# Kernel optimization log

Measured on AMD Instinct MI355X. Metric: run time of the kernel, lower is better.

## Reference

```python
import jax, jax.numpy as jnp
import numpy as np

B, Q, K, DQ, DK, H, DV = 4, 512, 512, 512, 512, 256, 512


def setup_inputs() -> dict:
    key = jax.random.key(0)
    ks = jax.random.split(key, 9)
    return {
        "query": jax.random.normal(ks[0], (B, Q, DQ), dtype=jnp.float32),
        "key": jax.random.normal(ks[1], (B, K, DK), dtype=jnp.float32),
        "value": jax.random.normal(ks[2], (B, K, DV), dtype=jnp.float32),
        "Wq": jax.random.normal(ks[3], (DQ, H), dtype=jnp.float32) / np.sqrt(DQ),
        "bq": jax.random.normal(ks[4], (H,), dtype=jnp.float32) * 0.01,
        "Wk": jax.random.normal(ks[5], (DK, H), dtype=jnp.float32) / np.sqrt(DK),
        "bk": jax.random.normal(ks[6], (H,), dtype=jnp.float32) * 0.01,
        "wv": jax.random.normal(ks[7], (H,), dtype=jnp.float32) / np.sqrt(H),
        "bv": jax.random.normal(ks[8], (), dtype=jnp.float32) * 0.01,
    }


def reference(query, key, value, Wq, bq, Wk, bk, wv, bv):
    # Projections: [B,Q,H] and [B,K,H]
    q = jnp.einsum("bqd,dh->bqh", query, Wq) + bq
    k = jnp.einsum("bkd,dh->bkh", key, Wk) + bk
    # Broadcast add + tanh: [B,Q,K,H] (the large intermediate)
    feat = jnp.tanh(q[:, :, None, :] + k[:, None, :, :])
    # Linear-to-scalar score: [B,Q,K]
    score = jnp.einsum("bqkh,h->bqk", feat, wv) + bv
    attention_weight = jax.nn.softmax(score, axis=-1)
    # Dropout is identity at eval; weighted sum over keys: [B,Q,DV]
    context = jnp.einsum("bqk,bkd->bqd", attention_weight, value)
    return (context, attention_weight)
```

## Files before the change

### kernel.cpp

```cpp
#include <hip/hip_runtime.h>
#include <hip/hip_bf16.h>

#define B_ 4
#define Q_ 512
#define K_ 512
#define DQ_ 512
#define H_ 256
#define DV_ 512

#define SC2 2.8853900817779268f

typedef unsigned short u16;
typedef short bf16x8 __attribute__((ext_vector_type(8)));
typedef float f32x4 __attribute__((ext_vector_type(4)));
typedef float f32x2 __attribute__((ext_vector_type(2)));
typedef unsigned short u16x4 __attribute__((ext_vector_type(4)));

__device__ __forceinline__ unsigned bsplit(float a) {
    unsigned u  = __float_as_uint(a);
    unsigned hi = (u + 0x7FFFu + ((u >> 16) & 1u)) >> 16;
    float hf = __uint_as_float(hi << 16);
    float l  = a - hf;
    unsigned ul = __float_as_uint(l);
    unsigned lo = (ul + 0x7FFFu + ((ul >> 16) & 1u)) >> 16;
    return (hi << 16) | lo;
}

__device__ __forceinline__ void gld16(const void* g, void* l) {
    __builtin_amdgcn_global_load_lds(
        (const __attribute__((address_space(1))) unsigned int*)g,
        (__attribute__((address_space(3))) unsigned int*)l, 16, 0, 0);
}

__device__ __forceinline__ void pair_acc(
    f32x2 Eq0, f32x2 Eq1, float ek0, float ek1,
    float w0, float w1, float w01, f32x2& acc)
{
    f32x2 e0 = Eq0 * (f32x2){ek0, ek0};
    f32x2 e1 = Eq1 * (f32x2){ek1, ek1};
    f32x2 s  = e0 + e1;
    f32x2 den = __builtin_elementwise_fma(e0, e1, s);
    den = den + (f32x2){1.f, 1.f};
    f32x2 num = __builtin_elementwise_fma(e1, (f32x2){w0, w0}, (f32x2){w01, w01});
    num = __builtin_elementwise_fma(e0, (f32x2){w1, w1}, num);
    f32x2 r = {__builtin_amdgcn_rcpf(den.x), __builtin_amdgcn_rcpf(den.y)};
    acc = __builtin_elementwise_fma(num, r, acc);
}

__global__ __launch_bounds__(256) void cvt_rows(
    const float* __restrict__ query, const float* __restrict__ key,
    u16* __restrict__ qA_hi, u16* __restrict__ qA_lo)
{
    const int z = blockIdx.y;
    const float* src = z ? key : query;
    u16* dh = qA_hi + (long long)z * 1048576;
    u16* dl = qA_lo + (long long)z * 1048576;
    long long i4 = (long long)blockIdx.x * 256 + threadIdx.x;
    float4 v = ((const float4*)src)[i4];
    unsigned a = bsplit(v.x), b = bsplit(v.y), c = bsplit(v.z), d = bsplit(v.w);
    u16x4 h4 = {(u16)(a >> 16), (u16)(b >> 16), (u16)(c >> 16), (u16)(d >> 16)};
    u16x4 l4 = {(u16)(a & 0xFFFF), (u16)(b & 0xFFFF), (u16)(c & 0xFFFF), (u16)(d & 0xFFFF)};
    *(u16x4*)(dh + i4 * 4) = h4;
    *(u16x4*)(dl + i4 * 4) = l4;
}

__global__ __launch_bounds__(256) void cvt_T(
    const float* __restrict__ Wq, const float* __restrict__ Wk,
    const float* __restrict__ value,
    u16* __restrict__ WT_hi, u16* __restrict__ WT_lo,
    u16* __restrict__ vT_hi, u16* __restrict__ vT_lo)
{
    __shared__ float t[32][33];
    const int z = blockIdx.z;
    const int x = threadIdx.x, y = threadIdx.y;
    const float* src; u16 *dh, *dl; int C;
    if (z < 2) {
        if (blockIdx.y >= 8) return;
        src = z ? Wk : Wq; C = 256;
        dh = WT_hi + (long long)z * 131072;
        dl = WT_lo + (long long)z * 131072;
    } else {
        src = value + (long long)(z - 2) * 262144; C = 512;
        dh = vT_hi + (long long)(z - 2) * 262144;
        dl = vT_lo + (long long)(z - 2) * 262144;
    }
    const int r0 = blockIdx.x * 32, c0 = blockIdx.y * 32;
    #pragma unroll
    for (int i = 0; i < 32; i += 8)
        t[y + i][x] = src[(long long)(r0 + y + i) * C + c0 + x];
    __syncthreads();
    #pragma unroll
    for (int i = 0; i < 32; i += 8) {
        unsigned p = bsplit(t[x][y + i]);
        long long o = (long long)(c0 + y + i) * 512 + r0 + x;
        dh[o] = (u16)(p >> 16);
        dl[o] = (u16)(p & 0xFFFF);
    }
}

__global__ __launch_bounds__(256) void mfma_gemm(
    const u16* __restrict__ Ah0, const u16* __restrict__ Al0,
    const u16* __restrict__ Bh0, const u16* __restrict__ Bl0,
    const float* __restrict__ biasq, const float* __restrict__ biask,
    float* __restrict__ outp, int mode, int Kd,
    long long sA, long long sB, long long sO)
{
    const int z = blockIdx.z;
    const u16* Ah = Ah0 + z * sA;
    const u16* Al = Al0 + z * sA;
    const u16* Bh = Bh0 + z * sB;
    const u16* Bl = Bl0 + z * sB;

    const int m0 = blockIdx.x * 64;
    const int n0 = blockIdx.y * 64;

    __shared__ u16 AhS[64 * 64], AlS[64 * 64], BhS[64 * 64], BlS[64 * 64];

    const int tid = threadIdx.x;
    const int lane = tid & 63, w = tid >> 6;
    const int wr = w >> 1, wc = w & 1;
    const int lrow = lane & 15, lgrp = lane >> 4;

    f32x4 acc[2][2] = {};

    for (int k0 = 0; k0 < Kd; k0 += 64) {
        #pragma unroll
        for (int it = 0; it < 2; ++it) {
            int idx = tid + it * 256;
            int row = idx >> 3, u = idx & 7;
            long long go = (long long)(m0 + row) * Kd + k0 + ((u ^ (row & 7)) << 3);
            long long gb = (long long)(n0 + row) * Kd + k0 + ((u ^ (row & 7)) << 3);
            gld16(Ah + go, AhS + idx * 8);
            gld16(Al + go, AlS + idx * 8);
            gld16(Bh + gb, BhS + idx * 8);
            gld16(Bl + gb, BlS + idx * 8);
        }
        __syncthreads();

        #pragma unroll
        for (int kk = 0; kk < 2; ++kk) {
            bf16x8 ah[2], al[2], bh[2], bl[2];
            #pragma unroll
            for (int f = 0; f < 2; ++f) {
                int ar = wr * 32 + f * 16 + lrow;
                int au = (kk * 4 + lgrp) ^ (ar & 7);
                ah[f] = *(const bf16x8*)(AhS + ar * 64 + au * 8);
                al[f] = *(const bf16x8*)(AlS + ar * 64 + au * 8);
                int br = wc * 32 + f * 16 + lrow;
                int bu = (kk * 4 + lgrp) ^ (br & 7);
                bh[f] = *(const bf16x8*)(BhS + br * 64 + bu * 8);
                bl[f] = *(const bf16x8*)(BlS + br * 64 + bu * 8);
            }
            #pragma unroll
            for (int fm = 0; fm < 2; ++fm)
                #pragma unroll
                for (int fn = 0; fn < 2; ++fn) {
                    acc[fm][fn] = __builtin_amdgcn_mfma_f32_16x16x32_bf16(ah[fm], bh[fn], acc[fm][fn], 0, 0, 0);
                    acc[fm][fn] = __builtin_amdgcn_mfma_f32_16x16x32_bf16(ah[fm], bl[fn], acc[fm][fn], 0, 0, 0);
                    acc[fm][fn] = __builtin_amdgcn_mfma_f32_16x16x32_bf16(al[fm], bh[fn], acc[fm][fn], 0, 0, 0);
                }
        }
        __syncthreads();
    }

    if (mode == 0) {
        const float* bs = z ? biask : biasq;
        #pragma unroll
        for (int fm = 0; fm < 2; ++fm)
            #pragma unroll
            for (int fn = 0; fn < 2; ++fn)
                #pragma unroll
                for (int r = 0; r < 4; ++r) {
                    int m = m0 + wr * 32 + fm * 16 + lgrp * 4 + r;
                    int n = n0 + wc * 32 + fn * 16 + lrow;
                    float v = __builtin_amdgcn_exp2f((acc[fm][fn][r] + bs[n]) * SC2);
                    if (z == 0) {
                        outp[(((long long)(m >> 2) * H_ + n) << 2) + (m & 3)] = v;
                    } else {
                        int bb = m >> 9, k = m & 511;
                        outp[sO + (((long long)(bb * 64 + (n >> 2)) * 512 + k) << 2) + (n & 3)] = v;
                    }
                }
    } else {
        float* C = outp + (long long)z * sO;
        #pragma unroll
        for (int fm = 0; fm < 2; ++fm)
            #pragma unroll
            for (int fn = 0; fn < 2; ++fn)
                #pragma unroll
                for (int r = 0; r < 4; ++r) {
                    int m = m0 + wr * 32 + fm * 16 + lgrp * 4 + r;
                    int n = n0 + wc * 32 + fn * 16 + lrow;
                    C[(long long)m * DV_ + n] = acc[fm][fn][r];
                }
    }
}

#define QT 4

__global__ __launch_bounds__(1024) void score_softmax(
    const float* __restrict__ qp4E,
    const float* __restrict__ kT4E,
    const float* __restrict__ wv,
    float* __restrict__ attn_out,
    u16* __restrict__ aB_hi, u16* __restrict__ aB_lo)
{
    const int b   = blockIdx.y;
    const int q0  = blockIdx.x * QT;
    const int tid = threadIdx.x;
    const int k16 = tid & 255;
    const int qtr = tid >> 8;
    const int lane = tid & 63;

    __shared__ float lq[H_][QT];
    __shared__ float lwp[H_ / 2][4];
    __shared__ float pacc[3][2][256][4];
    __shared__ float red[4][QT];

    if (tid < H_) {
        const float4* qsrc = (const float4*)qp4E + ((long long)(b * (Q_ / 4) + blockIdx.x)) * H_;
        *(float4*)&lq[tid][0] = qsrc[tid];
    } else if (tid < H_ + H_ / 2) {
        int p = tid - H_;
        float w0 = wv[2 * p], w1 = wv[2 * p + 1];
        lwp[p][0] = w0; lwp[p][1] = w1; lwp[p][2] = w0 + w1; lwp[p][3] = 0.f;
    }
    __syncthreads();

    f32x2 a01[2] = {{0.f,0.f},{0.f,0.f}}, a23[2] = {{0.f,0.f},{0.f,0.f}};
    const float4* kvec = (const float4*)kT4E + (long long)b * (H_ / 4) * K_ + k16;
    const int g0 = qtr * 16;

    float4 kA = kvec[(long long)g0 * K_];
    float4 kB = kvec[(long long)g0 * K_ + 256];
    #pragma unroll 2
    for (int gi = 0; gi < 16; ++gi) {
        const int g = g0 + gi;
        float4 kAc = kA, kBc = kB;
        if (gi < 15) {
            kA = kvec[(long long)(g + 1) * K_];
            kB = kvec[(long long)(g + 1) * K_ + 256];
        }
        float4 q4_0 = *(const float4*)&lq[(g << 2) + 0][0];
        float4 q4_1 = *(const float4*)&lq[(g << 2) + 1][0];
        float4 q4_2 = *(const float4*)&lq[(g << 2) + 2][0];
        float4 q4_3 = *(const float4*)&lq[(g << 2) + 3][0];
        float4 wp0 = *(const float4*)&lwp[(g << 1) + 0][0];
        float4 wp1 = *(const float4*)&lwp[(g << 1) + 1][0];

        f32x2 q0_01 = {q4_0.x, q4_0.y}, q0_23 = {q4_0.z, q4_0.w};
        f32x2 q1_01 = {q4_1.x, q4_1.y}, q1_23 = {q4_1.z, q4_1.w};
        f32x2 q2_01 = {q4_2.x, q4_2.y}, q2_23 = {q4_2.z, q4_2.w};
        f32x2 q3_01 = {q4_3.x, q4_3.y}, q3_23 = {q4_3.z, q4_3.w};

        pair_acc(q0_01, q1_01, kAc.x, kAc.y, wp0.x, wp0.y, wp0.z, a01[0]);
        pair_acc(q0_23, q1_23, kAc.x, kAc.y, wp0.x, wp0.y, wp0.z, a23[0]);
        pair_acc(q2_01, q3_01, kAc.z, kAc.w, wp1.x, wp1.y, wp1.z, a01[0]);
        pair_acc(q2_23, q3_23, kAc.z, kAc.w, wp1.x, wp1.y, wp1.z, a23[0]);
        pair_acc(q0_01, q1_01, kBc.x, kBc.y, wp0.x, wp0.y, wp0.z, a01[1]);
        pair_acc(q0_23, q1_23, kBc.x, kBc.y, wp0.x, wp0.y, wp0.z, a23[1]);
        pair_acc(q2_01, q3_01, kBc.z, kBc.w, wp1.x, wp1.y, wp1.z, a01[1]);
        pair_acc(q2_23, q3_23, kBc.z, kBc.w, wp1.x, wp1.y, wp1.z, a23[1]);
    }

    if (qtr) {
        #pragma unroll
        for (int kk = 0; kk < 2; ++kk) {
            float4 v = make_float4(a01[kk].x, a01[kk].y, a23[kk].x, a23[kk].y);
            *(float4*)&pacc[qtr - 1][kk][k16][0] = v;
        }
    }
    __syncthreads();

    float s[2][QT], e[2][QT], mx[QT];
    if (!qtr) {
        #pragma unroll
        for (int kk = 0; kk < 2; ++kk) {
            float4 t0 = *(const float4*)&pacc[0][kk][k16][0];
            float4 t1 = *(const float4*)&pacc[1][kk][k16][0];
            float4 t2 = *(const float4*)&pacc[2][kk][k16][0];
            s[kk][0] = -2.f * (a01[kk].x + t0.x + t1.x + t2.x);
            s[kk][1] = -2.f * (a01[kk].y + t0.y + t1.y + t2.y);
            s[kk][2] = -2.f * (a23[kk].x + t0.z + t1.z + t2.z);
            s[kk][3] = -2.f * (a23[kk].y + t0.w + t1.w + t2.w);
        }
        #pragma unroll
        for (int qq = 0; qq < QT; ++qq) {
            float v = fmaxf(s[0][qq], s[1][qq]);
            #pragma unroll
            for (int off = 32; off; off >>= 1) v = fmaxf(v, __shfl_xor(v, off));
            if (lane == 0) red[tid >> 6][qq] = v;
        }
    }
    __syncthreads();
    if (!qtr) {
        #pragma unroll
        for (int qq = 0; qq < QT; ++qq)
            mx[qq] = fmaxf(fmaxf(red[0][qq], red[1][qq]), fmaxf(red[2][qq], red[3][qq]));
    }
    __syncthreads();
    if (!qtr) {
        #pragma unroll
        for (int qq = 0; qq < QT; ++qq) {
            e[0][qq] = __expf(s[0][qq] - mx[qq]);
            e[1][qq] = __expf(s[1][qq] - mx[qq]);
            float v = e[0][qq] + e[1][qq];
            #pragma unroll
            for (int off = 32; off; off >>= 1) v += __shfl_xor(v, off);
            if (lane == 0) red[tid >> 6][qq] = v;
        }
    }
    __syncthreads();
    if (!qtr) {
        #pragma unroll
        for (int qq = 0; qq < QT; ++qq) {
            float v = red[0][qq] + red[1][qq] + red[2][qq] + red[3][qq];
            float rv = __builtin_amdgcn_rcpf(v);
            #pragma unroll
            for (int kk = 0; kk < 2; ++kk) {
                float a = e[kk][qq] * rv;
                long long o = (long long)(b * Q_ + q0 + qq) * K_ + k16 + kk * 256;
                attn_out[o] = a;
                unsigned p = bsplit(a);
                aB_hi[o] = (u16)(p >> 16);
                aB_lo[o] = (u16)(p & 0xFFFF);
            }
        }
    }
}

extern "C" void kernel_launch(void* const* d_in, const int* in_sizes, int n_in,
                              void* d_out, int out_size, void* d_ws, size_t ws_size,
                              hipStream_t stream) {
    const float* query = (const float*)d_in[0];
    const float* key   = (const float*)d_in[1];
    const float* value = (const float*)d_in[2];
    const float* Wq    = (const float*)d_in[3];
    const float* bq    = (const float*)d_in[4];
    const float* Wk    = (const float*)d_in[5];
    const float* bk    = (const float*)d_in[6];
    const float* wv    = (const float*)d_in[7];

    float* out = (float*)d_out;
    float* ctx_out  = out;
    float* attn_out = out + (size_t)B_ * Q_ * DV_;

    float* ws   = (float*)d_ws;
    float* qp4  = ws;
    float* kT4  = qp4 + 524288;
    u16* qA_hi  = (u16*)(kT4 + 524288);
    u16* kA_hi  = qA_hi + 1048576;
    u16* qA_lo  = kA_hi + 1048576;
    u16* kA_lo  = qA_lo + 1048576;
    u16* WqT_hi = kA_lo + 1048576;
    u16* WkT_hi = WqT_hi + 131072;
    u16* WqT_lo = WkT_hi + 131072;
    u16* WkT_lo = WqT_lo + 131072;
    u16* vT_hi  = WkT_lo + 131072;
    u16* vT_lo  = vT_hi + 1048576;
    u16* aB_hi  = vT_lo + 1048576;
    u16* aB_lo  = aB_hi + 1048576;
    (void)qA_lo; (void)WqT_lo; (void)n_in; (void)ws_size; (void)in_sizes; (void)out_size;

    hipLaunchKernelGGL(cvt_rows, dim3(1024, 2), dim3(256), 0, stream,
                       query, key, qA_hi, qA_lo);
    hipLaunchKernelGGL(cvt_T, dim3(16, 16, 6), dim3(32, 8), 0, stream,
                       Wq, Wk, value, WqT_hi, WqT_lo, vT_hi, vT_lo);

    hipLaunchKernelGGL(mfma_gemm, dim3(32, 4, 2), dim3(256), 0, stream,
                       qA_hi, qA_lo, WqT_hi, WqT_lo, bq, bk, qp4, 0, 512,
                       (long long)1048576, (long long)131072, (long long)524288);

    hipLaunchKernelGGL(score_softmax, dim3(Q_ / QT, B_), dim3(1024), 0, stream,
                       qp4, kT4, wv, attn_out, aB_hi, aB_lo);

    hipLaunchKernelGGL(mfma_gemm, dim3(8, 8, 4), dim3(256), 0, stream,
                       aB_hi, aB_lo, vT_hi, vT_lo, (const float*)nullptr, (const float*)nullptr,
                       ctx_out, 2, 512,
                       (long long)262144, (long long)262144, (long long)262144);
}
```

Before: 72.59 us.

## Merge conversion kernels, vectorize transpose stores, drop softmax max pass

Result: faster. 65.79 us (-9.4%).

```diff
diff --git a/kernel.cpp b/kernel.cpp
--- a/kernel.cpp
+++ b/kernel.cpp
@@ -47,35 +47,41 @@
     acc = __builtin_elementwise_fma(num, r, acc);
 }
 
-__global__ __launch_bounds__(256) void cvt_rows(
+__global__ __launch_bounds__(256) void prep_all(
     const float* __restrict__ query, const float* __restrict__ key,
-    u16* __restrict__ qA_hi, u16* __restrict__ qA_lo)
-{
-    const int z = blockIdx.y;
-    const float* src = z ? key : query;
-    u16* dh = qA_hi + (long long)z * 1048576;
-    u16* dl = qA_lo + (long long)z * 1048576;
-    long long i4 = (long long)blockIdx.x * 256 + threadIdx.x;
-    float4 v = ((const float4*)src)[i4];
-    unsigned a = bsplit(v.x), b = bsplit(v.y), c = bsplit(v.z), d = bsplit(v.w);
-    u16x4 h4 = {(u16)(a >> 16), (u16)(b >> 16), (u16)(c >> 16), (u16)(d >> 16)};
-    u16x4 l4 = {(u16)(a & 0xFFFF), (u16)(b & 0xFFFF), (u16)(c & 0xFFFF), (u16)(d & 0xFFFF)};
-    *(u16x4*)(dh + i4 * 4) = h4;
-    *(u16x4*)(dl + i4 * 4) = l4;
-}
-
-__global__ __launch_bounds__(256) void cvt_T(
     const float* __restrict__ Wq, const float* __restrict__ Wk,
     const float* __restrict__ value,
+    u16* __restrict__ qA_hi, u16* __restrict__ qA_lo,
     u16* __restrict__ WT_hi, u16* __restrict__ WT_lo,
     u16* __restrict__ vT_hi, u16* __restrict__ vT_lo)
 {
+    const int bx  = blockIdx.x;
+    const int tid = threadIdx.x;
+
+    if (bx < 2048) {
+        const int z = bx >> 10;
+        const float* src = z ? key : query;
+        u16* dh = qA_hi + (long long)z * 1048576;
+        u16* dl = qA_lo + (long long)z * 1048576;
+        long long i4 = (long long)(bx & 1023) * 256 + tid;
+        float4 v = ((const float4*)src)[i4];
+        unsigned a = bsplit(v.x), b = bsplit(v.y), c = bsplit(v.z), d = bsplit(v.w);
+        u16x4 h4 = {(u16)(a >> 16), (u16)(b >> 16), (u16)(c >> 16), (u16)(d >> 16)};
+        u16x4 l4 = {(u16)(a & 0xFFFF), (u16)(b & 0xFFFF), (u16)(c & 0xFFFF), (u16)(d & 0xFFFF)};
+        *(u16x4*)(dh + i4 * 4) = h4;
+        *(u16x4*)(dl + i4 * 4) = l4;
+        return;
+    }
+
     __shared__ float t[32][33];
-    const int z = blockIdx.z;
-    const int x = threadIdx.x, y = threadIdx.y;
+    const int flat = bx - 2048;
+    const int z  = flat >> 8;
+    const int rem = flat & 255;
+    const int gx = rem & 15, gy = rem >> 4;
+    const int x = tid & 31, y = tid >> 5;
     const float* src; u16 *dh, *dl; int C;
     if (z < 2) {
-        if (blockIdx.y >= 8) return;
+        if (gy >= 8) return;
         src = z ? Wk : Wq; C = 256;
         dh = WT_hi + (long long)z * 131072;
         dl = WT_lo + (long long)z * 131072;
@@ -84,17 +90,22 @@
         dh = vT_hi + (long long)(z - 2) * 262144;
         dl = vT_lo + (long long)(z - 2) * 262144;
     }
-    const int r0 = blockIdx.x * 32, c0 = blockIdx.y * 32;
+    const int r0 = gx * 32, c0 = gy * 32;
     #pragma unroll
     for (int i = 0; i < 32; i += 8)
         t[y + i][x] = src[(long long)(r0 + y + i) * C + c0 + x];
     __syncthreads();
-    #pragma unroll
-    for (int i = 0; i < 32; i += 8) {
-        unsigned p = bsplit(t[x][y + i]);
-        long long o = (long long)(c0 + y + i) * 512 + r0 + x;
-        dh[o] = (u16)(p >> 16);
-        dl[o] = (u16)(p & 0xFFFF);
+    {
+        const int r = tid >> 3, c = tid & 7;
+        unsigned p0 = bsplit(t[4 * c + 0][r]);
+        unsigned p1 = bsplit(t[4 * c + 1][r]);
+        unsigned p2 = bsplit(t[4 * c + 2][r]);
+        unsigned p3 = bsplit(t[4 * c + 3][r]);
+        long long o = (long long)(c0 + r) * 512 + r0 + 4 * c;
+        u16x4 h4 = {(u16)(p0 >> 16), (u16)(p1 >> 16), (u16)(p2 >> 16), (u16)(p3 >> 16)};
+        u16x4 l4 = {(u16)(p0 & 0xFFFF), (u16)(p1 & 0xFFFF), (u16)(p2 & 0xFFFF), (u16)(p3 & 0xFFFF)};
+        *(u16x4*)(dh + o) = h4;
+        *(u16x4*)(dl + o) = l4;
     }
 }
 
@@ -231,37 +242,52 @@
     const float4* kvec = (const float4*)kT4E + (long long)b * (H_ / 4) * K_ + k16;
     const int g0 = qtr * 16;
 
-    float4 kA = kvec[(long long)g0 * K_];
-    float4 kB = kvec[(long long)g0 * K_ + 256];
-    #pragma unroll 2
-    for (int gi = 0; gi < 16; ++gi) {
-        const int g = g0 + gi;
-        float4 kAc = kA, kBc = kB;
-        if (gi < 15) {
-            kA = kvec[(long long)(g + 1) * K_];
-            kB = kvec[(long long)(g + 1) * K_ + 256];
-        }
-        float4 q4_0 = *(const float4*)&lq[(g << 2) + 0][0];
-        float4 q4_1 = *(const float4*)&lq[(g << 2) + 1][0];
-        float4 q4_2 = *(const float4*)&lq[(g << 2) + 2][0];
-        float4 q4_3 = *(const float4*)&lq[(g << 2) + 3][0];
-        float4 wp0 = *(const float4*)&lwp[(g << 1) + 0][0];
-        float4 wp1 = *(const float4*)&lwp[(g << 1) + 1][0];
-
-        f32x2 q0_01 = {q4_0.x, q4_0.y}, q0_23 = {q4_0.z, q4_0.w};
-        f32x2 q1_01 = {q4_1.x, q4_1.y}, q1_23 = {q4_1.z, q4_1.w};
-        f32x2 q2_01 = {q4_2.x, q4_2.y}, q2_23 = {q4_2.z, q4_2.w};
-        f32x2 q3_01 = {q4_3.x, q4_3.y}, q3_23 = {q4_3.z, q4_3.w};
-
-        pair_acc(q0_01, q1_01, kAc.x, kAc.y, wp0.x, wp0.y, wp0.z, a01[0]);
-        pair_acc(q0_23, q1_23, kAc.x, kAc.y, wp0.x, wp0.y, wp0.z, a23[0]);
-        pair_acc(q2_01, q3_01, kAc.z, kAc.w, wp1.x, wp1.y, wp1.z, a01[0]);
-        pair_acc(q2_23, q3_23, kAc.z, kAc.w, wp1.x, wp1.y, wp1.z, a23[0]);
-        pair_acc(q0_01, q1_01, kBc.x, kBc.y, wp0.x, wp0.y, wp0.z, a01[1]);
-        pair_acc(q0_23, q1_23, kBc.x, kBc.y, wp0.x, wp0.y, wp0.z, a23[1]);
-        pair_acc(q2_01, q3_01, kBc.z, kBc.w, wp1.x, wp1.y, wp1.z, a01[1]);
-        pair_acc(q2_23, q3_23, kBc.z, kBc.w, wp1.x, wp1.y, wp1.z, a23[1]);
-    }
+#define SCORE_COMPUTE(GI, kAc, kBc) do {                                        \
+        const int g_ = g0 + (GI);                                               \
+        float4 q4_0 = *(const float4*)&lq[(g_ << 2) + 0][0];                    \
+        float4 q4_1 = *(const float4*)&lq[(g_ << 2) + 1][0];                    \
+        float4 q4_2 = *(const float4*)&lq[(g_ << 2) + 2][0];                    \
+        float4 q4_3 = *(const float4*)&lq[(g_ << 2) + 3][0];                    \
+        float4 wp0 = *(const float4*)&lwp[(g_ << 1) + 0][0];                    \
+        float4 wp1 = *(const float4*)&lwp[(g_ << 1) + 1][0];                    \
+        f32x2 q0_01 = {q4_0.x, q4_0.y}, q0_23 = {q4_0.z, q4_0.w};               \
+        f32x2 q1_01 = {q4_1.x, q4_1.y}, q1_23 = {q4_1.z, q4_1.w};               \
+        f32x2 q2_01 = {q4_2.x, q4_2.y}, q2_23 = {q4_2.z, q4_2.w};               \
+        f32x2 q3_01 = {q4_3.x, q4_3.y}, q3_23 = {q4_3.z, q4_3.w};               \
+        pair_acc(q0_01, q1_01, (kAc).x, (kAc).y, wp0.x, wp0.y, wp0.z, a01[0]);  \
+        pair_acc(q0_23, q1_23, (kAc).x, (kAc).y, wp0.x, wp0.y, wp0.z, a23[0]);  \
+        pair_acc(q2_01, q3_01, (kAc).z, (kAc).w, wp1.x, wp1.y, wp1.z, a01[0]);  \
+        pair_acc(q2_23, q3_23, (kAc).z, (kAc).w, wp1.x, wp1.y, wp1.z, a23[0]);  \
+        pair_acc(q0_01, q1_01, (kBc).x, (kBc).y, wp0.x, wp0.y, wp0.z, a01[1]);  \
+        pair_acc(q0_23, q1_23, (kBc).x, (kBc).y, wp0.x, wp0.y, wp0.z, a23[1]);  \
+        pair_acc(q2_01, q3_01, (kBc).z, (kBc).w, wp1.x, wp1.y, wp1.z, a01[1]);  \
+        pair_acc(q2_23, q3_23, (kBc).z, (kBc).w, wp1.x, wp1.y, wp1.z, a23[1]);  \
+    } while (0)
+
+    float4 A0 = kvec[(long long)(g0 + 0) * K_];
+    float4 B0 = kvec[(long long)(g0 + 0) * K_ + 256];
+    float4 A1 = kvec[(long long)(g0 + 1) * K_];
+    float4 B1 = kvec[(long long)(g0 + 1) * K_ + 256];
+    #pragma unroll
+    for (int gi = 0; gi < 16; gi += 2) {
+        {
+            float4 kAc = A0, kBc = B0;
+            if (gi + 2 < 16) {
+                A0 = kvec[(long long)(g0 + gi + 2) * K_];
+                B0 = kvec[(long long)(g0 + gi + 2) * K_ + 256];
+            }
+            SCORE_COMPUTE(gi, kAc, kBc);
+        }
+        {
+            float4 kAc = A1, kBc = B1;
+            if (gi + 3 < 16) {
+                A1 = kvec[(long long)(g0 + gi + 3) * K_];
+                B1 = kvec[(long long)(g0 + gi + 3) * K_ + 256];
+            }
+            SCORE_COMPUTE(gi + 1, kAc, kBc);
+        }
+    }
+#undef SCORE_COMPUTE
 
     if (qtr) {
         #pragma unroll
@@ -272,38 +298,24 @@
     }
     __syncthreads();
 
-    float s[2][QT], e[2][QT], mx[QT];
+    float e[2][QT];
     if (!qtr) {
         #pragma unroll
         for (int kk = 0; kk < 2; ++kk) {
             float4 t0 = *(const float4*)&pacc[0][kk][k16][0];
             float4 t1 = *(const float4*)&pacc[1][kk][k16][0];
             float4 t2 = *(const float4*)&pacc[2][kk][k16][0];
-            s[kk][0] = -2.f * (a01[kk].x + t0.x + t1.x + t2.x);
-            s[kk][1] = -2.f * (a01[kk].y + t0.y + t1.y + t2.y);
-            s[kk][2] = -2.f * (a23[kk].x + t0.z + t1.z + t2.z);
-            s[kk][3] = -2.f * (a23[kk].y + t0.w + t1.w + t2.w);
+            float at0 = a01[kk].x + t0.x + t1.x + t2.x;
+            float at1 = a01[kk].y + t0.y + t1.y + t2.y;
+            float at2 = a23[kk].x + t0.z + t1.z + t2.z;
+            float at3 = a23[kk].y + t0.w + t1.w + t2.w;
+            e[kk][0] = __builtin_amdgcn_exp2f(-SC2 * at0);
+            e[kk][1] = __builtin_amdgcn_exp2f(-SC2 * at1);
+            e[kk][2] = __builtin_amdgcn_exp2f(-SC2 * at2);
+            e[kk][3] = __builtin_amdgcn_exp2f(-SC2 * at3);
         }
         #pragma unroll
         for (int qq = 0; qq < QT; ++qq) {
-            float v = fmaxf(s[0][qq], s[1][qq]);
-            #pragma unroll
-            for (int off = 32; off; off >>= 1) v = fmaxf(v, __shfl_xor(v, off));
-            if (lane == 0) red[tid >> 6][qq] = v;
-        }
-    }
-    __syncthreads();
-    if (!qtr) {
-        #pragma unroll
-        for (int qq = 0; qq < QT; ++qq)
-            mx[qq] = fmaxf(fmaxf(red[0][qq], red[1][qq]), fmaxf(red[2][qq], red[3][qq]));
-    }
-    __syncthreads();
-    if (!qtr) {
-        #pragma unroll
-        for (int qq = 0; qq < QT; ++qq) {
-            e[0][qq] = __expf(s[0][qq] - mx[qq]);
-            e[1][qq] = __expf(s[1][qq] - mx[qq]);
             float v = e[0][qq] + e[1][qq];
             #pragma unroll
             for (int off = 32; off; off >>= 1) v += __shfl_xor(v, off);
@@ -362,10 +374,9 @@
     u16* aB_lo  = aB_hi + 1048576;
     (void)qA_lo; (void)WqT_lo; (void)n_in; (void)ws_size; (void)in_sizes; (void)out_size;
 
-    hipLaunchKernelGGL(cvt_rows, dim3(1024, 2), dim3(256), 0, stream,
-                       query, key, qA_hi, qA_lo);
-    hipLaunchKernelGGL(cvt_T, dim3(16, 16, 6), dim3(32, 8), 0, stream,
-                       Wq, Wk, value, WqT_hi, WqT_lo, vT_hi, vT_lo);
+    hipLaunchKernelGGL(prep_all, dim3(3584), dim3(256), 0, stream,
+                       query, key, Wq, Wk, value,
+                       qA_hi, qA_lo, WqT_hi, WqT_lo, vT_hi, vT_lo);
 
     hipLaunchKernelGGL(mfma_gemm, dim3(32, 4, 2), dim3(256), 0, stream,
                        qA_hi, qA_lo, WqT_hi, WqT_lo, bq, bk, qp4, 0, 512,
```
